# Kernel optimization log

Hardware: AMD Instinct MI355X
Metric: run time of the kernel (lower is better)

## Reference

```python
import jax, jax.numpy as jnp
import numpy as np

SIG = 1000  # signal length hard-coded in the torch module

def _fourier_weights(n, conj):
    k, m = np.mgrid[0:n, 0:n]
    theta = 2.0 * np.pi * k * m / n
    sin_sign = 1.0 if conj else -1.0
    return np.hstack([np.cos(theta), sin_sign * np.sin(theta)]).astype(np.float32)  # (n, 2n)

def setup_inputs() -> dict:
    key = jax.random.key(0)
    k_x, k_w3, k_b3 = jax.random.split(key, 3)
    x = jax.random.normal(k_x, (8192, SIG), dtype=jnp.float32)
    filters = jnp.asarray(np.hamming(SIG), dtype=jnp.float32)[None, :]        # (1, 1000)
    Wf = jnp.asarray(_fourier_weights(SIG, conj=False))                        # (1000, 2000)
    Wfc = jnp.asarray(_fourier_weights(SIG, conj=True))                        # (1000, 2000)
    W3 = jax.random.normal(k_w3, (141, 500), dtype=jnp.float32)                # fc3 weight
    b3 = jax.random.normal(k_b3, (141,), dtype=jnp.float32) * 0.01             # fc3 bias
    return {"x": x, "filters": filters, "Wf": Wf, "Wfc": Wfc, "W3": W3, "b3": b3}

def reference(x, filters, Wf, Wfc, W3, b3):
    ham = x * filters                              # windowed signal, (B, 1000)
    out = ham @ Wf                                 # (B, 2000): [real | imag] of DFT
    out2 = ham @ Wfc                               # (B, 2000): [real | imag] of conj-DFT
    r1, i1 = out[:, :SIG], out[:, SIG:]
    r2, i2 = out2[:, :SIG], out2[:, SIG:]
    # |fft * fftconj| / 1000^2
    pr = r1 * r2 - i1 * i2
    pi = r1 * i2 + i1 * r2
    psd = jnp.sqrt(pr * pr + pi * pi) / (SIG ** 2)
    freq_probs = psd[:, :500] @ W3.T + b3          # (B, 141)
    return freq_probs
```

## Files before the change

kernel.cpp:

```cpp
#include <hip/hip_runtime.h>
#include <hip/hip_bf16.h>

#define SIG   1000
#define MROWS 8192
#define FK    512
#define FW    1024
#define NPAD  1024
#define PSDK  512
#define HN    192
#define NOUT  141
#define NT    16

using f32x4  = __attribute__((ext_vector_type(4))) float;
using short8 = __attribute__((ext_vector_type(8))) short;

__device__ inline ushort f2bf(float f) {
  union { float f; unsigned u; } v; v.f = f;
  unsigned u = v.u;
  unsigned r = (u + 0x7FFFu + ((u >> 16) & 1u)) >> 16;
  return (ushort)r;
}

#define SYNC_BOUNDARY(WAITSTR)                         \
  do {                                                 \
    __builtin_amdgcn_sched_barrier(0);                 \
    asm volatile(WAITSTR ::: "memory");                \
    __builtin_amdgcn_s_barrier();                      \
    __builtin_amdgcn_sched_barrier(0);                 \
  } while (0)

__global__ __launch_bounds__(256) void prep_k(
    const float* __restrict__ x, const float* __restrict__ filt,
    const float* __restrict__ W3, ushort* __restrict__ fh,
    ushort* __restrict__ Bt, ushort* __restrict__ W3p) {
  const int tid = threadIdx.x;
  const int blk = blockIdx.x;
  if (blk < MROWS / 2) {
    const int r = blk * 2 + (tid >> 7);
    const int c = tid & 127;
    ushort4 e = make_ushort4(0, 0, 0, 0);
    ushort4 o = make_ushort4(0, 0, 0, 0);
    if (c < 125) {
      const float4* xr = (const float4*)(x + (size_t)r * SIG);
      const float4* fr = (const float4*)filt;
      const float4 xl = xr[c],       fl = fr[c];
      const float4 xh = xr[c + 125], fv = fr[c + 125];
      float lx = xl.x * fl.x, ly = xl.y * fl.y, lz = xl.z * fl.z, lw = xl.w * fl.w;
      float hx = xh.x * fv.x, hy = xh.y * fv.y, hz = xh.z * fv.z, hw = xh.w * fv.w;
      e.x = f2bf(lx + hx); e.y = f2bf(ly + hy); e.z = f2bf(lz + hz); e.w = f2bf(lw + hw);
      o.x = f2bf(lx - hx); o.y = f2bf(ly - hy); o.z = f2bf(lz - hz); o.w = f2bf(lw - hw);
    }
    ((ushort4*)(fh + (size_t)r * FW))[c]      = e;
    ((ushort4*)(fh + (size_t)r * FW + FK))[c] = o;
  } else {
    const int row = (blk - MROWS / 2) * 2 + (tid >> 7);
    const int c   = tid & 127;
    if (row < NPAD) {
      const int cg = row & 511, g = row >> 9;
      ushort4 o = make_ushort4(0, 0, 0, 0);
      if (cg < 500) {
        const int m = 2 * (cg >> 1) + g;
        const int trig = cg & 1;
        const float C = 6.28318530717958647692f / 1000.0f;
        ushort v[4];
#pragma unroll
        for (int j = 0; j < 4; ++j) {
          int ph = ((4 * c + j) * m) % 1000;
          float ang = ph * C;
          v[j] = f2bf(trig ? __sinf(ang) : __cosf(ang));
        }
        o = make_ushort4(v[0], v[1], v[2], v[3]);
      }
      ((ushort4*)(Bt + (size_t)row * FK))[c] = o;
    } else {
      const int n = row - NPAD;
      ushort4 o = make_ushort4(0, 0, 0, 0);
      if (n < NOUT && c < 125) {
        const float4 w = *(const float4*)(W3 + (size_t)n * 500 + 4 * c);
        o.x = f2bf(w.x); o.y = f2bf(w.y); o.z = f2bf(w.z); o.w = f2bf(w.w);
      }
      ((ushort4*)(W3p + (size_t)n * PSDK))[c] = o;
    }
  }
}

__global__ __launch_bounds__(512, 4) void gemm_psd_k(
    const ushort* __restrict__ A, const ushort* __restrict__ Bt,
    ushort* __restrict__ psd) {
  __shared__ ushort lA[3][128 * 32];
  __shared__ ushort lB[3][128 * 32];
  const int tid  = threadIdx.x;
  const int wave = tid >> 6;
  const int lane = tid & 63;
  const int id  = blockIdx.x;
  const int xcd = id & 7, rr = id >> 3;
  const int bx  = xcd * 8 + (rr & 7);
  const int by  = rr >> 3;
  const int row0 = bx * 128;
  const int n0   = by * 128;
  const int aoff = (by >= 4) ? FK : 0;
  const int wm = (wave >> 1) * 32;
  const int wn = (wave & 1) * 64;
  const int lr = lane & 15;
  const int kg = (lane >> 4) * 8;

  const int doff = wave * 1024;
  const int soff = doff + lane * 16;
  const int srow = soff >> 6;
  const int skb  = (soff & 63) >> 1;
  const ushort* gA = A  + (size_t)(row0 + srow) * FW + aoff + skb;
  const ushort* gB = Bt + (size_t)(n0   + srow) * FK + skb;

  auto STAGE = [&](int buf, int k0) {
    __builtin_amdgcn_global_load_lds(
        (const __attribute__((address_space(1))) void*)(gA + k0),
        (__attribute__((address_space(3))) void*)((char*)lA[buf] + doff), 16, 0, 0);
    __builtin_amdgcn_global_load_lds(
        (const __attribute__((address_space(1))) void*)(gB + k0),
        (__attribute__((address_space(3))) void*)((char*)lB[buf] + doff), 16, 0, 0);
  };

  f32x4 acc[2][4] = {};

  STAGE(0, 0);
  STAGE(1, 32);
  SYNC_BOUNDARY("s_waitcnt vmcnt(2)");

#pragma unroll
  for (int kt = 0; kt < NT; ++kt) {
    const int cur = kt % 3;
    if (kt + 2 < NT) STAGE((kt + 2) % 3, (kt + 2) * 32);
    short8 a[2], b[4];
    const ushort* baseA = lA[cur];
    const ushort* baseB = lB[cur];
#pragma unroll
    for (int m = 0; m < 2; ++m)
      a[m] = *(const short8*)&baseA[(wm + m * 16 + lr) * 32 + kg];
#pragma unroll
    for (int n = 0; n < 4; ++n)
      b[n] = *(const short8*)&baseB[(wn + n * 16 + lr) * 32 + kg];
#pragma unroll
    for (int m = 0; m < 2; ++m)
#pragma unroll
      for (int n = 0; n < 4; ++n)
        acc[m][n] = __builtin_amdgcn_mfma_f32_16x16x32_bf16(a[m], b[n], acc[m][n], 0, 0, 0);
    if (kt < NT - 1) {
      if (kt + 2 < NT)
        SYNC_BOUNDARY("s_waitcnt vmcnt(2) lgkmcnt(0)");
      else
        SYNC_BOUNDARY("s_waitcnt vmcnt(0) lgkmcnt(0)");
    }
  }

  const int g = by >> 2;
  const int colpar = lane & 1;
#pragma unroll
  for (int m = 0; m < 2; ++m) {
#pragma unroll
    for (int n = 0; n < 4; ++n) {
#pragma unroll
      for (int j = 0; j < 4; ++j) {
        float v  = acc[m][n][j];
        float v2 = __shfl_xor(v, 1);
        if (!colpar) {
          int grow = row0 + wm + m * 16 + (lane >> 4) * 4 + j;
          int cg   = ((n0 + wn + n * 16 + lr) & 511);
          int mbin = (cg & ~1) + g;
          psd[(size_t)grow * PSDK + mbin] = f2bf((v * v + v2 * v2) * 1e-6f);
        }
      }
    }
  }
}

__global__ __launch_bounds__(256, 2) void head_gemm_k(
    const ushort* __restrict__ psd, const ushort* __restrict__ W3p,
    const float* __restrict__ b3, float* __restrict__ out) {
  __shared__ ushort lA[3][16 * 32];
  __shared__ ushort lB[3][HN * 32];
  const int tid  = threadIdx.x;
  const int wave = tid >> 6;
  const int lane = tid & 63;
  const int row0 = blockIdx.x * 16;
  const int wn = wave * 48;
  const int lr = lane & 15;
  const int kg = (lane >> 4) * 8;

  const ushort* gs[4];
  int doff[4], isa[4], valid[4];
#pragma unroll
  for (int j = 0; j < 4; ++j) {
    const int i = wave + 4 * j;
    valid[j] = (i < 13);
    const int ia  = (i == 0);
    const int idx = ia ? 0 : (i - 1);
    const int off = (ia ? 0 : idx * 1024) + lane * 16;
    const int row = off >> 6;
    const int kb  = (off & 63) >> 1;
    gs[j]   = ia ? (psd + (size_t)(row0 + row) * PSDK + kb)
                 : (W3p + (size_t)row * PSDK + kb);
    doff[j] = ia ? 0 : idx * 1024;
    isa[j]  = ia;
  }

  auto HSTAGE = [&](int buf, int k0) {
#pragma unroll
    for (int j = 0; j < 4; ++j) {
      if (valid[j]) {
        char* db = (isa[j] ? (char*)lA[buf] : (char*)lB[buf]) + doff[j];
        __builtin_amdgcn_global_load_lds(
            (const __attribute__((address_space(1))) void*)(gs[j] + k0),
            (__attribute__((address_space(3))) void*)db, 16, 0, 0);
      }
    }
  };

  f32x4 acc[3] = {};

  HSTAGE(0, 0);
  HSTAGE(1, 32);
  __builtin_amdgcn_sched_barrier(0);
  if (wave == 0) asm volatile("s_waitcnt vmcnt(4)" ::: "memory");
  else           asm volatile("s_waitcnt vmcnt(3)" ::: "memory");
  __builtin_amdgcn_s_barrier();
  __builtin_amdgcn_sched_barrier(0);

#pragma unroll
  for (int kt = 0; kt < NT; ++kt) {
    const int cur = kt % 3;
    if (kt + 2 < NT) HSTAGE((kt + 2) % 3, (kt + 2) * 32);
    short8 a, b[3];
    const ushort* baseA = lA[cur];
    const ushort* baseB = lB[cur];
    a = *(const short8*)&baseA[lr * 32 + kg];
#pragma unroll
    for (int n = 0; n < 3; ++n)
      b[n] = *(const short8*)&baseB[(wn + n * 16 + lr) * 32 + kg];
#pragma unroll
    for (int n = 0; n < 3; ++n)
      acc[n] = __builtin_amdgcn_mfma_f32_16x16x32_bf16(a, b[n], acc[n], 0, 0, 0);
    if (kt < NT - 1) {
      __builtin_amdgcn_sched_barrier(0);
      if (kt + 2 < NT) {
        if (wave == 0) asm volatile("s_waitcnt vmcnt(4) lgkmcnt(0)" ::: "memory");
        else           asm volatile("s_waitcnt vmcnt(3) lgkmcnt(0)" ::: "memory");
      } else {
        asm volatile("s_waitcnt vmcnt(0) lgkmcnt(0)" ::: "memory");
      }
      __builtin_amdgcn_s_barrier();
      __builtin_amdgcn_sched_barrier(0);
    }
  }

#pragma unroll
  for (int n = 0; n < 3; ++n) {
#pragma unroll
    for (int j = 0; j < 4; ++j) {
      int gcol = wn + n * 16 + lr;
      if (gcol < NOUT) {
        int grow = row0 + (lane >> 4) * 4 + j;
        out[(size_t)grow * NOUT + gcol] = acc[n][j] + b3[gcol];
      }
    }
  }
}

extern "C" void kernel_launch(void* const* d_in, const int* in_sizes, int n_in,
                              void* d_out, int out_size, void* d_ws, size_t ws_size,
                              hipStream_t stream) {
  const float* x    = (const float*)d_in[0];
  const float* filt = (const float*)d_in[1];
  const float* W3   = (const float*)d_in[4];
  const float* b3   = (const float*)d_in[5];
  float* out = (float*)d_out;

  char* ws = (char*)d_ws;
  ushort* fh  = (ushort*)ws;
  ushort* Bt  = (ushort*)(ws + (size_t)MROWS * FW * 2);
  ushort* psd = (ushort*)(ws + (size_t)MROWS * FW * 2
                             + (size_t)NPAD * FK * 2);
  ushort* W3p = (ushort*)(ws + (size_t)MROWS * FW * 2
                             + (size_t)NPAD * FK * 2
                             + (size_t)MROWS * PSDK * 2);

  prep_k<<<MROWS / 2 + (NPAD + HN) / 2, 256, 0, stream>>>(x, filt, W3, fh, Bt, W3p);
  gemm_psd_k<<<(MROWS / 128) * (NPAD / 128), 512, 0, stream>>>(fh, Bt, psd);
  head_gemm_k<<<MROWS / 16, 256, 0, stream>>>(psd, W3p, b3, out);
}
```

Baseline: 36.35 us.

## Fuse windowing and even/odd fold of x into the DFT GEMM A-tile load

Drops the separate pass that windowed x, folded it into even/odd halves and wrote a bf16 buffer. The DFT GEMM now loads fp32 x directly into registers, applies the Hamming filter from LDS, forms the sum or difference in-kernel, and writes the bf16 A tile to LDS. Register double-buffering and retuned vmcnt waits keep the loads pipelined. This removes a 16 MB intermediate write and its read-back. In exchange the GEMM reads fp32 x redundantly across the 8 column blocks, uses more registers, and puts extra ALU work and LDS stores on the critical loop.

```diff
diff --git a/kernel.cpp b/kernel.cpp
--- a/kernel.cpp
+++ b/kernel.cpp
@@ -4,7 +4,6 @@
 #define SIG   1000
 #define MROWS 8192
 #define FK    512
-#define FW    1024
 #define NPAD  1024
 #define PSDK  512
 #define HN    192
@@ -17,78 +16,52 @@
 __device__ inline ushort f2bf(float f) {
   union { float f; unsigned u; } v; v.f = f;
   unsigned u = v.u;
-  unsigned r = (u + 0x7FFFu + ((u >> 16) & 1u)) >> 16;
-  return (ushort)r;
-}
-
-#define SYNC_BOUNDARY(WAITSTR)                         \
-  do {                                                 \
-    __builtin_amdgcn_sched_barrier(0);                 \
-    asm volatile(WAITSTR ::: "memory");                \
-    __builtin_amdgcn_s_barrier();                      \
-    __builtin_amdgcn_sched_barrier(0);                 \
-  } while (0)
-
-__global__ __launch_bounds__(256) void prep_k(
+  return (ushort)((u + 0x7FFFu + ((u >> 16) & 1u)) >> 16);
+}
+__device__ inline uint pk2(float a, float b) {
+  return (uint)f2bf(a) | ((uint)f2bf(b) << 16);
+}
+#define SB0() __builtin_amdgcn_sched_barrier(0)
+
+__global__ __launch_bounds__(256) void wprep_k(
+    const float* __restrict__ W3, ushort* __restrict__ Bt,
+    ushort* __restrict__ W3p) {
+  const int row = blockIdx.x * 2 + (threadIdx.x >> 7);
+  const int c   = threadIdx.x & 127;
+  if (row < NPAD) {
+    const int cg = row & 511, g = row >> 9;
+    ushort4 o = make_ushort4(0, 0, 0, 0);
+    if (cg < 500) {
+      const int m = 2 * (cg >> 1) + g;
+      const int trig = cg & 1;
+      const float C = 6.28318530717958647692f / 1000.0f;
+      ushort v[4];
+#pragma unroll
+      for (int j = 0; j < 4; ++j) {
+        int ph = ((4 * c + j) * m) % 1000;
+        float ang = ph * C;
+        v[j] = f2bf(trig ? __sinf(ang) : __cosf(ang));
+      }
+      o = make_ushort4(v[0], v[1], v[2], v[3]);
+    }
+    ((ushort4*)(Bt + (size_t)row * FK))[c] = o;
+  } else {
+    const int n = row - NPAD;
+    ushort4 o = make_ushort4(0, 0, 0, 0);
+    if (n < NOUT && c < 125) {
+      const float4 w = *(const float4*)(W3 + (size_t)n * 500 + 4 * c);
+      o.x = f2bf(w.x); o.y = f2bf(w.y); o.z = f2bf(w.z); o.w = f2bf(w.w);
+    }
+    ((ushort4*)(W3p + (size_t)n * PSDK))[c] = o;
+  }
+}
+
+__global__ __launch_bounds__(512, 4) void gemm_psd_k(
     const float* __restrict__ x, const float* __restrict__ filt,
-    const float* __restrict__ W3, ushort* __restrict__ fh,
-    ushort* __restrict__ Bt, ushort* __restrict__ W3p) {
-  const int tid = threadIdx.x;
-  const int blk = blockIdx.x;
-  if (blk < MROWS / 2) {
-    const int r = blk * 2 + (tid >> 7);
-    const int c = tid & 127;
-    ushort4 e = make_ushort4(0, 0, 0, 0);
-    ushort4 o = make_ushort4(0, 0, 0, 0);
-    if (c < 125) {
-      const float4* xr = (const float4*)(x + (size_t)r * SIG);
-      const float4* fr = (const float4*)filt;
-      const float4 xl = xr[c],       fl = fr[c];
-      const float4 xh = xr[c + 125], fv = fr[c + 125];
-      float lx = xl.x * fl.x, ly = xl.y * fl.y, lz = xl.z * fl.z, lw = xl.w * fl.w;
-      float hx = xh.x * fv.x, hy = xh.y * fv.y, hz = xh.z * fv.z, hw = xh.w * fv.w;
-      e.x = f2bf(lx + hx); e.y = f2bf(ly + hy); e.z = f2bf(lz + hz); e.w = f2bf(lw + hw);
-      o.x = f2bf(lx - hx); o.y = f2bf(ly - hy); o.z = f2bf(lz - hz); o.w = f2bf(lw - hw);
-    }
-    ((ushort4*)(fh + (size_t)r * FW))[c]      = e;
-    ((ushort4*)(fh + (size_t)r * FW + FK))[c] = o;
-  } else {
-    const int row = (blk - MROWS / 2) * 2 + (tid >> 7);
-    const int c   = tid & 127;
-    if (row < NPAD) {
-      const int cg = row & 511, g = row >> 9;
-      ushort4 o = make_ushort4(0, 0, 0, 0);
-      if (cg < 500) {
-        const int m = 2 * (cg >> 1) + g;
-        const int trig = cg & 1;
-        const float C = 6.28318530717958647692f / 1000.0f;
-        ushort v[4];
-#pragma unroll
-        for (int j = 0; j < 4; ++j) {
-          int ph = ((4 * c + j) * m) % 1000;
-          float ang = ph * C;
-          v[j] = f2bf(trig ? __sinf(ang) : __cosf(ang));
-        }
-        o = make_ushort4(v[0], v[1], v[2], v[3]);
-      }
-      ((ushort4*)(Bt + (size_t)row * FK))[c] = o;
-    } else {
-      const int n = row - NPAD;
-      ushort4 o = make_ushort4(0, 0, 0, 0);
-      if (n < NOUT && c < 125) {
-        const float4 w = *(const float4*)(W3 + (size_t)n * 500 + 4 * c);
-        o.x = f2bf(w.x); o.y = f2bf(w.y); o.z = f2bf(w.z); o.w = f2bf(w.w);
-      }
-      ((ushort4*)(W3p + (size_t)n * PSDK))[c] = o;
-    }
-  }
-}
-
-__global__ __launch_bounds__(512, 4) void gemm_psd_k(
-    const ushort* __restrict__ A, const ushort* __restrict__ Bt,
-    ushort* __restrict__ psd) {
+    const ushort* __restrict__ Bt, ushort* __restrict__ psd) {
   __shared__ ushort lA[3][128 * 32];
   __shared__ ushort lB[3][128 * 32];
+  __shared__ float  fp[1024];
   const int tid  = threadIdx.x;
   const int wave = tid >> 6;
   const int lane = tid & 63;
@@ -98,38 +71,85 @@
   const int by  = rr >> 3;
   const int row0 = bx * 128;
   const int n0   = by * 128;
-  const int aoff = (by >= 4) ? FK : 0;
+  const bool neg = (by >= 4);
   const int wm = (wave >> 1) * 32;
   const int wn = (wave & 1) * 64;
   const int lr = lane & 15;
   const int kg = (lane >> 4) * 8;
 
-  const int doff = wave * 1024;
-  const int soff = doff + lane * 16;
-  const int srow = soff >> 6;
-  const int skb  = (soff & 63) >> 1;
-  const ushort* gA = A  + (size_t)(row0 + srow) * FW + aoff + skb;
-  const ushort* gB = Bt + (size_t)(n0   + srow) * FK + skb;
-
-  auto STAGE = [&](int buf, int k0) {
-    __builtin_amdgcn_global_load_lds(
-        (const __attribute__((address_space(1))) void*)(gA + k0),
-        (__attribute__((address_space(3))) void*)((char*)lA[buf] + doff), 16, 0, 0);
+  const int arow = tid >> 2;
+  const int kq   = tid & 3;
+  const float* xlo = x + (size_t)(row0 + arow) * SIG + kq * 8;
+  const float* xhi = xlo + 500;
+  const float* xsafe = x + (size_t)(row0 + arow) * SIG + 992;
+  const float* fpa = fp + kq * 8;
+  const float* fpb = fp + 512 + kq * 8;
+
+  const int doffB = wave * 1024;
+  const int soffB = doffB + lane * 16;
+  const int srowB = soffB >> 6, skbB = (soffB & 63) >> 1;
+  const ushort* gB = Bt + (size_t)(n0 + srowB) * FK + skbB;
+
+  auto STAGE_B = [&](int buf, int k0) {
     __builtin_amdgcn_global_load_lds(
         (const __attribute__((address_space(1))) void*)(gB + k0),
-        (__attribute__((address_space(3))) void*)((char*)lB[buf] + doff), 16, 0, 0);
+        (__attribute__((address_space(3))) void*)((char*)lB[buf] + doffB), 16, 0, 0);
   };
+  auto ISSUE_X = [&](float4* d, int t) {
+    d[0] = *(const float4*)(xlo + t * 32);
+    d[1] = *(const float4*)(xlo + t * 32 + 4);
+    if (t == 15) {
+      d[2] = *(const float4*)((kq <= 2) ? (xhi + 480) : xsafe);
+      d[3] = *(const float4*)((kq <= 1) ? (xhi + 484) : xsafe);
+    } else {
+      d[2] = *(const float4*)(xhi + t * 32);
+      d[3] = *(const float4*)(xhi + t * 32 + 4);
+    }
+  };
+  auto FOLD = [&](const float4* d, int t, int buf) {
+    const float4 fa0 = *(const float4*)(fpa + t * 32);
+    const float4 fa1 = *(const float4*)(fpa + t * 32 + 4);
+    const float4 fb0 = *(const float4*)(fpb + t * 32);
+    const float4 fb1 = *(const float4*)(fpb + t * 32 + 4);
+    float o[8];
+#pragma unroll
+    for (int j = 0; j < 4; ++j) {
+      float lo0 = d[0][j] * fa0[j], p0 = d[2][j] * fb0[j];
+      float lo1 = d[1][j] * fa1[j], p1 = d[3][j] * fb1[j];
+      o[j]     = neg ? (lo0 - p0) : (lo0 + p0);
+      o[4 + j] = neg ? (lo1 - p1) : (lo1 + p1);
+    }
+    uint4 v = make_uint4(pk2(o[0], o[1]), pk2(o[2], o[3]),
+                         pk2(o[4], o[5]), pk2(o[6], o[7]));
+    *(uint4*)&lA[buf][arow * 32 + kq * 8] = v;
+  };
 
   f32x4 acc[2][4] = {};
-
-  STAGE(0, 0);
-  STAGE(1, 32);
-  SYNC_BOUNDARY("s_waitcnt vmcnt(2)");
+  float4 xa[4], xb[4];
+
+  fp[tid]       = (tid < 500) ? filt[tid]       : 0.f;
+  fp[tid + 512] = (tid < 500) ? filt[tid + 500] : 0.f;
+  ISSUE_X(xa, 0); STAGE_B(0, 0);
+  SB0();
+  ISSUE_X(xb, 1); STAGE_B(1, 32);
+  SB0(); asm volatile("s_waitcnt lgkmcnt(0)" ::: "memory");
+  __builtin_amdgcn_s_barrier(); SB0();
+  SB0(); asm volatile("s_waitcnt vmcnt(5)" ::: "memory"); SB0();
+  FOLD(xa, 0, 0);
+  SB0(); asm volatile("s_waitcnt lgkmcnt(0)" ::: "memory");
+  __builtin_amdgcn_s_barrier(); SB0();
 
 #pragma unroll
   for (int kt = 0; kt < NT; ++kt) {
     const int cur = kt % 3;
-    if (kt + 2 < NT) STAGE((kt + 2) % 3, (kt + 2) * 32);
+    float4* dst = (kt & 1) ? xb : xa;
+    const float4* src = (kt & 1) ? xa : xb;
+    if (kt + 2 < NT) { ISSUE_X(dst, kt + 2); STAGE_B((kt + 2) % 3, (kt + 2) * 32); }
+    SB0();
+    if (kt <= 13)      asm volatile("s_waitcnt vmcnt(6)" ::: "memory");
+    else if (kt == 14) asm volatile("s_waitcnt vmcnt(1)" ::: "memory");
+    SB0();
+    if (kt + 1 < NT) FOLD(src, kt + 1, (kt + 1) % 3);
     short8 a[2], b[4];
     const ushort* baseA = lA[cur];
     const ushort* baseB = lB[cur];
@@ -145,10 +165,11 @@
       for (int n = 0; n < 4; ++n)
         acc[m][n] = __builtin_amdgcn_mfma_f32_16x16x32_bf16(a[m], b[n], acc[m][n], 0, 0, 0);
     if (kt < NT - 1) {
-      if (kt + 2 < NT)
-        SYNC_BOUNDARY("s_waitcnt vmcnt(2) lgkmcnt(0)");
-      else
-        SYNC_BOUNDARY("s_waitcnt vmcnt(0) lgkmcnt(0)");
+      SB0();
+      if (kt <= 13) asm volatile("s_waitcnt vmcnt(5) lgkmcnt(0)" ::: "memory");
+      else          asm volatile("s_waitcnt vmcnt(0) lgkmcnt(0)" ::: "memory");
+      __builtin_amdgcn_s_barrier();
+      SB0();
     }
   }
 
@@ -202,7 +223,6 @@
     doff[j] = ia ? 0 : idx * 1024;
     isa[j]  = ia;
   }
-
   auto HSTAGE = [&](int buf, int k0) {
 #pragma unroll
     for (int j = 0; j < 4; ++j) {
@@ -216,14 +236,13 @@
   };
 
   f32x4 acc[3] = {};
-
   HSTAGE(0, 0);
   HSTAGE(1, 32);
-  __builtin_amdgcn_sched_barrier(0);
+  SB0();
   if (wave == 0) asm volatile("s_waitcnt vmcnt(4)" ::: "memory");
   else           asm volatile("s_waitcnt vmcnt(3)" ::: "memory");
   __builtin_amdgcn_s_barrier();
-  __builtin_amdgcn_sched_barrier(0);
+  SB0();
 
 #pragma unroll
   for (int kt = 0; kt < NT; ++kt) {
@@ -240,7 +259,7 @@
     for (int n = 0; n < 3; ++n)
       acc[n] = __builtin_amdgcn_mfma_f32_16x16x32_bf16(a, b[n], acc[n], 0, 0, 0);
     if (kt < NT - 1) {
-      __builtin_amdgcn_sched_barrier(0);
+      SB0();
       if (kt + 2 < NT) {
         if (wave == 0) asm volatile("s_waitcnt vmcnt(4) lgkmcnt(0)" ::: "memory");
         else           asm volatile("s_waitcnt vmcnt(3) lgkmcnt(0)" ::: "memory");
@@ -248,7 +267,7 @@
         asm volatile("s_waitcnt vmcnt(0) lgkmcnt(0)" ::: "memory");
       }
       __builtin_amdgcn_s_barrier();
-      __builtin_amdgcn_sched_barrier(0);
+      SB0();
     }
   }
 
@@ -275,15 +294,12 @@
   float* out = (float*)d_out;
 
   char* ws = (char*)d_ws;
-  ushort* fh  = (ushort*)ws;
-  ushort* Bt  = (ushort*)(ws + (size_t)MROWS * FW * 2);
-  ushort* psd = (ushort*)(ws + (size_t)MROWS * FW * 2
-                             + (size_t)NPAD * FK * 2);
-  ushort* W3p = (ushort*)(ws + (size_t)MROWS * FW * 2
-                             + (size_t)NPAD * FK * 2
+  ushort* Bt  = (ushort*)ws;
+  ushort* psd = (ushort*)(ws + (size_t)NPAD * FK * 2);
+  ushort* W3p = (ushort*)(ws + (size_t)NPAD * FK * 2
                              + (size_t)MROWS * PSDK * 2);
 
-  prep_k<<<MROWS / 2 + (NPAD + HN) / 2, 256, 0, stream>>>(x, filt, W3, fh, Bt, W3p);
-  gemm_psd_k<<<(MROWS / 128) * (NPAD / 128), 512, 0, stream>>>(fh, Bt, psd);
+  wprep_k<<<(NPAD + HN) / 2, 256, 0, stream>>>(W3, Bt, W3p);
+  gemm_psd_k<<<(MROWS / 128) * (NPAD / 128), 512, 0, stream>>>(x, filt, Bt, psd);
   head_gemm_k<<<MROWS / 16, 256, 0, stream>>>(psd, W3p, b3, out);
 }
```

After: 46.92 us. 1.29x slower.
